# Performance work log

Measured on AMD Instinct MI355X. Metric: run time of the kernel, lower is better.

## Reference

```python
import jax, jax.numpy as jnp
import numpy as np

L = 5        # n_layers
H = 8        # heads
DH = 32      # dim_head = n_hidden // heads
D = 256      # n_hidden
KR = 4       # key_ratio
QKD = KR * DH  # 128, q/k feature dim
IN = 3       # fun_dim + space_dim
OUT = 1      # out_dim
N = 32768    # number of mesh points
EPS = 1e-5

def _ln(x, g, b):
    m = jnp.mean(x, axis=-1, keepdims=True)
    v = jnp.var(x, axis=-1, keepdims=True)
    return (x - m) * jax.lax.rsqrt(v + EPS) * g + b

def _gelu(x):
    return jax.nn.gelu(x, approximate=False)  # torch nn.GELU default (erf)

def setup_inputs() -> dict:
    key = jax.random.key(0)
    ks = iter(jax.random.split(key, 64))
    def w(*s):
        return jax.random.normal(next(ks), s, jnp.float32) * 0.02
    return {
        "x": jax.random.normal(next(ks), (N, IN), jnp.float32),
        # preprocess MLP: Linear(IN,2D)+GELU, Linear(2D,D)
        "pre_w1": w(IN, 2 * D), "pre_b1": jnp.zeros((2 * D,), jnp.float32),
        "pre_w2": w(2 * D, D), "pre_b2": jnp.zeros((D,), jnp.float32),
        "placeholder": jax.random.uniform(next(ks), (D,), jnp.float32) / D,
        # per-block params stacked over L
        "ln1_g": jnp.ones((L, D), jnp.float32), "ln1_b": jnp.zeros((L, D), jnp.float32),
        "inp_w": w(L, D, D), "inp_b": jnp.zeros((L, D), jnp.float32),
        "temp_q": jnp.full((L, H), 0.5, jnp.float32), "temp_k": jnp.full((L, H), 0.5, jnp.float32),
        "wq": w(L, DH, QKD), "wk": w(L, DH, QKD), "wv": w(L, DH, DH),
        "out_w1": w(L, D, D), "out_b1": jnp.zeros((L, D), jnp.float32),
        "out_w2": w(L, D, D), "out_b2": jnp.zeros((L, D), jnp.float32),
        "ln2_g": jnp.ones((L, D), jnp.float32), "ln2_b": jnp.zeros((L, D), jnp.float32),
        "mlp_w1": w(L, D, D), "mlp_b1": jnp.zeros((L, D), jnp.float32),  # mlp_ratio=1 -> hidden=D
        "mlp_w2": w(L, D, D), "mlp_b2": jnp.zeros((L, D), jnp.float32),
        # last-layer head
        "ln3_g": jnp.ones((D,), jnp.float32), "ln3_b": jnp.zeros((D,), jnp.float32),
        "head_w": w(D, OUT), "head_b": jnp.zeros((OUT,), jnp.float32),
    }

def reference(x, pre_w1, pre_b1, pre_w2, pre_b2, placeholder,
              ln1_g, ln1_b, inp_w, inp_b, temp_q, temp_k, wq, wk, wv,
              out_w1, out_b1, out_w2, out_b2, ln2_g, ln2_b,
              mlp_w1, mlp_b1, mlp_w2, mlp_b2, ln3_g, ln3_b, head_w, head_b):
    # preprocess + placeholder bias
    fx = _gelu(x[None] @ pre_w1 + pre_b1) @ pre_w2 + pre_b2  # [1, N, D]
    fx = fx + placeholder
    for i in range(L):
        # --- LinearNO attention block ---
        h = _ln(fx, ln1_g[i], ln1_b[i])
        xm = h @ inp_w[i] + inp_b[i]                       # [1, N, D]
        xm = xm.reshape(1, N, H, DH).transpose(0, 2, 1, 3)  # [1, H, N, DH]
        q = jnp.einsum('bhnd,de->bhne', xm, wq[i])          # [1, H, N, QKD]
        k = jnp.einsum('bhnd,de->bhne', xm, wk[i])          # [1, H, N, QKD]
        v = jnp.einsum('bhnd,dc->bhnc', xm, wv[i])          # [1, H, N, DH]
        tq = jnp.clip(temp_q[i], 0.1, 2.0)[None, :, None, None]
        tk = jnp.clip(temp_k[i], 0.1, 2.0)[None, :, None, None]
        q = jax.nn.softmax(q / tq, axis=-1)  # over feature dim
        k = jax.nn.softmax(k / tk, axis=-2)  # over point dim
        kv = jnp.einsum('bhnd,bhnc->bhdc', k, v)    # [1, H, QKD, DH]
        qkv = jnp.einsum('bhnd,bhdc->bhnc', q, kv)  # [1, H, N, DH]
        qkv = qkv.transpose(0, 2, 1, 3).reshape(1, N, D)
        attn = _gelu(qkv @ out_w1[i] + out_b1[i]) @ out_w2[i] + out_b2[i]
        fx = attn + fx
        # --- MLP block (n_layers=0, res=False: pre + post only) ---
        h2 = _ln(fx, ln2_g[i], ln2_b[i])
        fx = _gelu(h2 @ mlp_w1[i] + mlp_b1[i]) @ mlp_w2[i] + mlp_b2[i] + fx
    # last block head: mlp2(ln_3(fx))
    out = _ln(fx, ln3_g, ln3_b) @ head_w + head_b  # [1, N, OUT]
    return out[0]  # module returns fx[0]
```

## Files before the change

### kernel.cpp

```cpp
#include <hip/hip_runtime.h>
#include <hip/hip_bf16.h>
#include <math.h>

constexpr int NP  = 32768;
constexpr int HH  = 8;

typedef short bf16x8 __attribute__((ext_vector_type(8)));
typedef float f32x4  __attribute__((ext_vector_type(4)));

__device__ __forceinline__ float gelu_f(float x) {
    return 0.5f * x * (1.0f + erff(x * 0.70710678118654752f));
}

__device__ __forceinline__ unsigned short f2bf(float x) {
    union { float f; unsigned u; } v; v.f = x;
    unsigned r = v.u + 0x7fffu + ((v.u >> 16) & 1u);
    return (unsigned short)(r >> 16);
}

__device__ __forceinline__ float bf2f(unsigned short h) {
    union { unsigned u; float f; } v; v.u = ((unsigned)h) << 16;
    return v.f;
}

__global__ __launch_bounds__(256) void transpose_bf16_k(
    const float* __restrict__ src, unsigned short* __restrict__ dst, int K)
{
    __shared__ float tile[32][33];
    int g = blockIdx.z;
    int k0 = blockIdx.x * 32, c0 = blockIdx.y * 32;
    int tx = threadIdx.x & 31, ty = threadIdx.x >> 5;
    const float* s = src + (size_t)g * K * 256;
    unsigned short* d = dst + (size_t)g * 256 * K;
    #pragma unroll
    for (int rr = 0; rr < 4; ++rr) {
        int r = ty + rr * 8;
        tile[r][tx] = s[(size_t)(k0 + r) * 256 + c0 + tx];
    }
    __syncthreads();
    #pragma unroll
    for (int rr = 0; rr < 4; ++rr) {
        int r = ty + rr * 8;
        d[(size_t)(c0 + r) * K + k0 + tx] = f2bf(tile[tx][r]);
    }
}

__global__ __launch_bounds__(256) void transpose_scale_bf16_k(
    const float* __restrict__ src, const float* __restrict__ g,
    unsigned short* __restrict__ dst, int K)
{
    __shared__ float tile[32][33];
    int z = blockIdx.z;
    int k0 = blockIdx.x * 32, c0 = blockIdx.y * 32;
    int tx = threadIdx.x & 31, ty = threadIdx.x >> 5;
    const float* s = src + (size_t)z * K * 256;
    unsigned short* d = dst + (size_t)z * 256 * K;
    #pragma unroll
    for (int rr = 0; rr < 4; ++rr) {
        int r = ty + rr * 8;
        tile[r][tx] = s[(size_t)(k0 + r) * 256 + c0 + tx];
    }
    __syncthreads();
    float gs = g[z * 256 + k0 + tx];
    #pragma unroll
    for (int rr = 0; rr < 4; ++rr) {
        int r = ty + rr * 8;
        d[(size_t)(c0 + r) * K + k0 + tx] = f2bf(gs * tile[tx][r]);
    }
}

__global__ __launch_bounds__(256) void colsum_k(
    const float* __restrict__ W, const float* __restrict__ g,
    const float* __restrict__ b, float* __restrict__ c2, float* __restrict__ c1)
{
    int z = blockIdx.z, c = threadIdx.x;
    const float* Wz = W + (size_t)z * 65536;
    const float* gz = g + z * 256;
    const float* bz = b + z * 256;
    float s2 = 0.f, s1 = 0.f;
    for (int k = 0; k < 256; ++k) {
        float w = Wz[k * 256 + c];
        s2 += gz[k] * w;
        s1 += bz[k] * w;
    }
    c2[z * 256 + c] = s2;
    c1[z * 256 + c] = s1;
}

__global__ __launch_bounds__(256) void prep_wkvT(
    const float* __restrict__ wk, const float* __restrict__ wv,
    const float* __restrict__ wq,
    unsigned short* __restrict__ wkT, unsigned short* __restrict__ wvT,
    unsigned short* __restrict__ wqT)
{
    int l = blockIdx.x, tid = threadIdx.x;
    for (int idx = tid; idx < 4096; idx += 256) {
        int d = idx >> 5, k = idx & 31;
        wkT[l * 4096 + idx] = f2bf(wk[l * 4096 + k * 128 + d]);
        wqT[l * 4096 + idx] = f2bf(wq[l * 4096 + k * 128 + d]);
    }
    for (int idx = tid; idx < 1024; idx += 256) {
        int c = idx >> 5, k = idx & 31;
        wvT[l * 1024 + idx] = f2bf(wv[l * 1024 + k * 32 + c]);
    }
}

template<bool GENA, bool AF32, bool LNFOLD, bool DOGELU, bool RESID, bool STATS, bool PERM>
__global__ __launch_bounds__(256) void gemm_bf(
    const unsigned short* __restrict__ Ah, const float* __restrict__ Af,
    const unsigned short* __restrict__ Wt,
    const float* __restrict__ bias, const float* __restrict__ bias2,
    float* __restrict__ outF, unsigned short* __restrict__ outH,
    const float* __restrict__ stats_in, float* __restrict__ stats_out,
    const float* __restrict__ c1v, const float* __restrict__ c2vec,
    const float* __restrict__ genx, const float* __restrict__ genw1,
    const float* __restrict__ genb1, int K)
{
    __shared__ __align__(16) unsigned short As[128 * 64];
    __shared__ __align__(16) unsigned short Bs[128 * 64];
    __shared__ float rmean[LNFOLD ? 128 : 1];
    __shared__ float rrstd[LNFOLD ? 128 : 1];
    __shared__ float w1s[GENA ? 1536 : 1];
    __shared__ float b1s[GENA ? 512 : 1];
    __shared__ float x3s[GENA ? 512 : 1];

    const int tid = threadIdx.x;
    const int rBase = blockIdx.x * 128, cBase = blockIdx.y * 128;

    if constexpr (GENA) {
        for (int i2 = tid; i2 < 1536; i2 += 256) w1s[i2] = genw1[i2];
        for (int i2 = tid; i2 < 512; i2 += 256) b1s[i2] = genb1[i2];
        if (tid < 128) {
            x3s[tid * 4 + 0] = genx[(size_t)(rBase + tid) * 3 + 0];
            x3s[tid * 4 + 1] = genx[(size_t)(rBase + tid) * 3 + 1];
            x3s[tid * 4 + 2] = genx[(size_t)(rBase + tid) * 3 + 2];
        }
        __syncthreads();
    }
    if constexpr (LNFOLD) {
        if (tid < 128) {
            const float* sp = stats_in + (size_t)(rBase + tid) * 8;
            float4 s0 = *(const float4*)sp;
            float4 s1 = *(const float4*)(sp + 4);
            float mean = (s0.x + s0.z + s1.x + s1.z) * (1.f / 256.f);
            float ex2  = (s0.y + s0.w + s1.y + s1.w) * (1.f / 256.f);
            rmean[tid] = mean;
            rrstd[tid] = rsqrtf(fmaxf(ex2 - mean * mean, 0.f) + 1e-5f);
        }
        __syncthreads();
    }

    f32x4 acc[4][4];
    #pragma unroll
    for (int i = 0; i < 4; ++i)
        #pragma unroll
        for (int j = 0; j < 4; ++j)
            acc[i][j] = (f32x4){0.f, 0.f, 0.f, 0.f};

    const int lane = tid & 63, wid = tid >> 6;
    const int wr = wid >> 1, wc = wid & 1;
    const int lrow = lane & 15, quad = lane >> 4;
    const int srow = tid >> 3;
    const int sch  = tid & 7;

    for (int kc = 0; kc < K; kc += 64) {
        if constexpr (GENA) {
            #pragma unroll
            for (int it = 0; it < 4; ++it) {
                int row = srow + it * 32;
                float x0 = x3s[row * 4 + 0], x1 = x3s[row * 4 + 1], x2 = x3s[row * 4 + 2];
                unsigned short pk[8];
                #pragma unroll
                for (int j = 0; j < 8; ++j) {
                    int k = kc + sch * 8 + j;
                    float t = x0 * w1s[k] + x1 * w1s[512 + k] + x2 * w1s[1024 + k] + b1s[k];
                    pk[j] = f2bf(gelu_f(t));
                }
                *(uint4*)&As[row * 64 + ((sch ^ (row & 7)) << 3)] = *(uint4*)pk;
            }
        } else if constexpr (AF32) {
            #pragma unroll
            for (int it = 0; it < 4; ++it) {
                int row = srow + it * 32;
                const float* ap = Af + (size_t)(rBase + row) * K + kc + sch * 8;
                float4 a0 = *(const float4*)ap;
                float4 a1 = *(const float4*)(ap + 4);
                unsigned short pk[8];
                pk[0] = f2bf(a0.x); pk[1] = f2bf(a0.y); pk[2] = f2bf(a0.z); pk[3] = f2bf(a0.w);
                pk[4] = f2bf(a1.x); pk[5] = f2bf(a1.y); pk[6] = f2bf(a1.z); pk[7] = f2bf(a1.w);
                *(uint4*)&As[row * 64 + ((sch ^ (row & 7)) << 3)] = *(uint4*)pk;
            }
        } else {
            #pragma unroll
            for (int it = 0; it < 4; ++it) {
                int row = srow + it * 32;
                uint4 av = *(const uint4*)(Ah + (size_t)(rBase + row) * K + kc + sch * 8);
                *(uint4*)&As[row * 64 + ((sch ^ (row & 7)) << 3)] = av;
            }
        }
        #pragma unroll
        for (int it = 0; it < 4; ++it) {
            int n = srow + it * 32;
            uint4 wv_ = *(const uint4*)(Wt + (size_t)(cBase + n) * K + kc + sch * 8);
            *(uint4*)&Bs[n * 64 + ((sch ^ (n & 7)) << 3)] = wv_;
        }
        __syncthreads();
        #pragma unroll
        for (int ks = 0; ks < 2; ++ks) {
            bf16x8 af[4], bfr[4];
            #pragma unroll
            for (int t = 0; t < 4; ++t) {
                int row = wr * 64 + t * 16 + lrow;
                af[t] = *(bf16x8*)&As[row * 64 + (((ks * 4 + quad) ^ (row & 7)) << 3)];
                int n = wc * 64 + t * 16 + lrow;
                bfr[t] = *(bf16x8*)&Bs[n * 64 + (((ks * 4 + quad) ^ (n & 7)) << 3)];
            }
            #pragma unroll
            for (int ti = 0; ti < 4; ++ti)
                #pragma unroll
                for (int tj = 0; tj < 4; ++tj)
                    acc[ti][tj] = __builtin_amdgcn_mfma_f32_16x16x32_bf16(
                        af[ti], bfr[tj], acc[ti][tj], 0, 0, 0);
        }
        __syncthreads();
    }

    float c1b[4], c2r[4];
    #pragma unroll
    for (int tj = 0; tj < 4; ++tj) {
        int gcol = cBase + wc * 64 + tj * 16 + lrow;
        float b = bias[gcol];
        if (bias2) b += bias2[gcol];
        if constexpr (LNFOLD) {
            c1b[tj] = c1v[gcol] + b;
            c2r[tj] = c2vec[gcol];
        } else {
            c1b[tj] = b;
            c2r[tj] = 0.f;
        }
    }
    #pragma unroll
    for (int ti = 0; ti < 4; ++ti) {
        #pragma unroll
        for (int r = 0; r < 4; ++r) {
            int rib = wr * 64 + ti * 16 + quad * 4 + r;
            int grow = rBase + rib;
            float mean = 0.f, rstd = 1.f;
            if constexpr (LNFOLD) { mean = rmean[rib]; rstd = rrstd[rib]; }
            float vv[4];
            #pragma unroll
            for (int tj = 0; tj < 4; ++tj) {
                float t = acc[ti][tj][r];
                float v;
                if constexpr (LNFOLD) v = rstd * (t - mean * c2r[tj]) + c1b[tj];
                else                  v = t + c1b[tj];
                if constexpr (DOGELU) v = gelu_f(v);
                vv[tj] = v;
            }
            if constexpr (RESID) {
                #pragma unroll
                for (int tj = 0; tj < 4; ++tj) {
                    int gcol = cBase + wc * 64 + tj * 16 + lrow;
                    vv[tj] += outF[(size_t)grow * 256 + gcol];
                }
            }
            if constexpr (STATS) {
                float rs = vv[0] + vv[1] + vv[2] + vv[3];
                float rq = vv[0]*vv[0] + vv[1]*vv[1] + vv[2]*vv[2] + vv[3]*vv[3];
                #pragma unroll
                for (int m = 1; m < 16; m <<= 1) {
                    rs += __shfl_xor(rs, m);
                    rq += __shfl_xor(rq, m);
                }
                if (lrow == 0) {
                    stats_out[(size_t)grow * 8 + (blockIdx.y * 2 + wc) * 2 + 0] = rs;
                    stats_out[(size_t)grow * 8 + (blockIdx.y * 2 + wc) * 2 + 1] = rq;
                }
            }
            #pragma unroll
            for (int tj = 0; tj < 4; ++tj) {
                int gcol = cBase + wc * 64 + tj * 16 + lrow;
                if constexpr (PERM) {
                    size_t pidx = (size_t)(gcol >> 5) * NP * 32 + (size_t)grow * 32 + (gcol & 31);
                    if (outF) outF[pidx] = vv[tj];
                    if (outH) outH[pidx] = f2bf(vv[tj]);
                } else {
                    if (outF) outF[(size_t)grow * 256 + gcol] = vv[tj];
                    if (outH) outH[(size_t)grow * 256 + gcol] = f2bf(vv[tj]);
                }
            }
        }
    }
}

template<bool AF32, bool LNFOLD, bool WSTATS, bool NEXTW>
__global__ __launch_bounds__(256) void gemm_lgl(
    const unsigned short* __restrict__ Ah, const float* __restrict__ Af,
    const unsigned short* __restrict__ W1t, const unsigned short* __restrict__ W2t,
    const float* __restrict__ b1, const float* __restrict__ b2,
    float* __restrict__ fx,
    const float* __restrict__ stats_in, float* __restrict__ stats_out,
    const float* __restrict__ c1v, const float* __restrict__ c2vec,
    const unsigned short* __restrict__ W3t, const float* __restrict__ b3,
    const float* __restrict__ c1n, const float* __restrict__ c2n,
    unsigned short* __restrict__ outNext)
{
    __shared__ __align__(16) unsigned short As[64 * 64];
    __shared__ __align__(16) unsigned short Bs[256 * 64];
    __shared__ __align__(16) unsigned short Ts[64 * 256];
    __shared__ float rmean[(LNFOLD || NEXTW) ? 64 : 1];
    __shared__ float rrstd[(LNFOLD || NEXTW) ? 64 : 1];
    __shared__ float ssum[NEXTW ? 256 : 1];
    __shared__ float ssq [NEXTW ? 256 : 1];

    const int tid = threadIdx.x;
    const int rBase = blockIdx.x * 64;
    const int lane = tid & 63, wid = tid >> 6;
    const int lrow = lane & 15, quad = lane >> 4;

    if constexpr (LNFOLD) {
        if (tid < 64) {
            const float* sp = stats_in + (size_t)(rBase + tid) * 8;
            float4 s0 = *(const float4*)sp;
            float4 s1 = *(const float4*)(sp + 4);
            float mean = (s0.x + s0.z + s1.x + s1.z) * (1.f / 256.f);
            float ex2  = (s0.y + s0.w + s1.y + s1.w) * (1.f / 256.f);
            rmean[tid] = mean;
            rrstd[tid] = rsqrtf(fmaxf(ex2 - mean * mean, 0.f) + 1e-5f);
        }
    }

    f32x4 acc[4][4];
    #pragma unroll
    for (int i = 0; i < 4; ++i)
        #pragma unroll
        for (int j = 0; j < 4; ++j)
            acc[i][j] = (f32x4){0.f, 0.f, 0.f, 0.f};

    for (int kc = 0; kc < 256; kc += 64) {
        #pragma unroll
        for (int it = 0; it < 2; ++it) {
            int idx = tid + it * 256;
            int row = idx >> 3, sch = idx & 7;
            if constexpr (AF32) {
                const float* ap = Af + (size_t)(rBase + row) * 256 + kc + sch * 8;
                float4 a0 = *(const float4*)ap;
                float4 a1 = *(const float4*)(ap + 4);
                unsigned short pk[8];
                pk[0] = f2bf(a0.x); pk[1] = f2bf(a0.y); pk[2] = f2bf(a0.z); pk[3] = f2bf(a0.w);
                pk[4] = f2bf(a1.x); pk[5] = f2bf(a1.y); pk[6] = f2bf(a1.z); pk[7] = f2bf(a1.w);
                *(uint4*)&As[row * 64 + ((sch ^ (row & 7)) << 3)] = *(uint4*)pk;
            } else {
                uint4 av = *(const uint4*)(Ah + (size_t)(rBase + row) * 256 + kc + sch * 8);
                *(uint4*)&As[row * 64 + ((sch ^ (row & 7)) << 3)] = av;
            }
        }
        #pragma unroll
        for (int it = 0; it < 8; ++it) {
            int idx = tid + it * 256;
            int n = idx >> 3, sch = idx & 7;
            uint4 wv_ = *(const uint4*)(W1t + (size_t)n * 256 + kc + sch * 8);
            *(uint4*)&Bs[n * 64 + ((sch ^ (n & 7)) << 3)] = wv_;
        }
        __syncthreads();
        #pragma unroll
        for (int ks = 0; ks < 2; ++ks) {
            bf16x8 af[4], bfr[4];
            #pragma unroll
            for (int t = 0; t < 4; ++t) {
                int row = t * 16 + lrow;
                af[t] = *(bf16x8*)&As[row * 64 + (((ks * 4 + quad) ^ (row & 7)) << 3)];
                int n = wid * 64 + t * 16 + lrow;
                bfr[t] = *(bf16x8*)&Bs[n * 64 + (((ks * 4 + quad) ^ (n & 7)) << 3)];
            }
            #pragma unroll
            for (int ti = 0; ti < 4; ++ti)
                #pragma unroll
                for (int tj = 0; tj < 4; ++tj)
                    acc[ti][tj] = __builtin_amdgcn_mfma_f32_16x16x32_bf16(
                        af[ti], bfr[tj], acc[ti][tj], 0, 0, 0);
        }
        __syncthreads();
    }

    {
        float c1b[4], c2r[4];
        #pragma unroll
        for (int tj = 0; tj < 4; ++tj) {
            int gcol = wid * 64 + tj * 16 + lrow;
            if constexpr (LNFOLD) {
                c1b[tj] = c1v[gcol] + b1[gcol];
                c2r[tj] = c2vec[gcol];
            } else {
                c1b[tj] = b1[gcol];
                c2r[tj] = 0.f;
            }
        }
        #pragma unroll
        for (int ti = 0; ti < 4; ++ti) {
            #pragma unroll
            for (int r = 0; r < 4; ++r) {
                int row = ti * 16 + quad * 4 + r;
                float mean = 0.f, rstd = 1.f;
                if constexpr (LNFOLD) { mean = rmean[row]; rstd = rrstd[row]; }
                #pragma unroll
                for (int tj = 0; tj < 4; ++tj) {
                    float t = acc[ti][tj][r];
                    float v;
                    if constexpr (LNFOLD) v = rstd * (t - mean * c2r[tj]) + c1b[tj];
                    else                  v = t + c1b[tj];
                    v = gelu_f(v);
                    int col = wid * 64 + tj * 16 + lrow;
                    int ch = col >> 3;
                    Ts[row * 256 + ((ch ^ (row & 7)) << 3) + (col & 7)] = f2bf(v);
                }
            }
        }
    }
    __syncthreads();

    f32x4 acc2[4][4];
    #pragma unroll
    for (int i = 0; i < 4; ++i)
        #pragma unroll
        for (int j = 0; j < 4; ++j)
            acc2[i][j] = (f32x4){0.f, 0.f, 0.f, 0.f};

    for (int kc = 0; kc < 256; kc += 64) {
        #pragma unroll
        for (int it = 0; it < 8; ++it) {
            int idx = tid + it * 256;
            int n = idx >> 3, sch = idx & 7;
            uint4 wv_ = *(const uint4*)(W2t + (size_t)n * 256 + kc + sch * 8);
            *(uint4*)&Bs[n * 64 + ((sch ^ (n & 7)) << 3)] = wv_;
        }
        __syncthreads();
        #pragma unroll
        for (int ks = 0; ks < 2; ++ks) {
            bf16x8 af[4], bfr[4];
            #pragma unroll
            for (int t = 0; t < 4; ++t) {
                int row = t * 16 + lrow;
                int ch = (kc >> 3) + ks * 4 + quad;
                af[t] = *(bf16x8*)&Ts[row * 256 + ((ch ^ (row & 7)) << 3)];
                int n = wid * 64 + t * 16 + lrow;
                bfr[t] = *(bf16x8*)&Bs[n * 64 + (((ks * 4 + quad) ^ (n & 7)) << 3)];
            }
            #pragma unroll
            for (int ti = 0; ti < 4; ++ti)
                #pragma unroll
                for (int tj = 0; tj < 4; ++tj)
                    acc2[ti][tj] = __builtin_amdgcn_mfma_f32_16x16x32_bf16(
                        af[ti], bfr[tj], acc2[ti][tj], 0, 0, 0);
        }
        __syncthreads();
    }

    float bb[4];
    #pragma unroll
    for (int tj = 0; tj < 4; ++tj) bb[tj] = b2[wid * 64 + tj * 16 + lrow];
    #pragma unroll
    for (int ti = 0; ti < 4; ++ti) {
        #pragma unroll
        for (int r = 0; r < 4; ++r) {
            int row = ti * 16 + quad * 4 + r;
            int grow = rBase + row;
            float vv[4];
            #pragma unroll
            for (int tj = 0; tj < 4; ++tj) {
                int gcol = wid * 64 + tj * 16 + lrow;
                vv[tj] = acc2[ti][tj][r] + bb[tj] + fx[(size_t)grow * 256 + gcol];
            }
            if constexpr (WSTATS || NEXTW) {
                float rs = vv[0] + vv[1] + vv[2] + vv[3];
                float rq = vv[0]*vv[0] + vv[1]*vv[1] + vv[2]*vv[2] + vv[3]*vv[3];
                #pragma unroll
                for (int m = 1; m < 16; m <<= 1) {
                    rs += __shfl_xor(rs, m);
                    rq += __shfl_xor(rq, m);
                }
                if (lrow == 0) {
                    if constexpr (WSTATS) {
                        stats_out[(size_t)grow * 8 + wid * 2 + 0] = rs;
                        stats_out[(size_t)grow * 8 + wid * 2 + 1] = rq;
                    }
                    if constexpr (NEXTW) {
                        ssum[row * 4 + wid] = rs;
                        ssq [row * 4 + wid] = rq;
                    }
                }
            }
            #pragma unroll
            for (int tj = 0; tj < 4; ++tj) {
                int gcol = wid * 64 + tj * 16 + lrow;
                fx[(size_t)grow * 256 + gcol] = vv[tj];
                if constexpr (NEXTW) {
                    int ch = gcol >> 3;
                    Ts[row * 256 + ((ch ^ (row & 7)) << 3) + (gcol & 7)] = f2bf(vv[tj]);
                }
            }
        }
    }

    if constexpr (NEXTW) {
        __syncthreads();
        if (tid < 64) {
            float q0 = ssum[tid * 4 + 0], q1 = ssum[tid * 4 + 1];
            float q2 = ssum[tid * 4 + 2], q3 = ssum[tid * 4 + 3];
            float p0 = ssq [tid * 4 + 0], p1 = ssq [tid * 4 + 1];
            float p2 = ssq [tid * 4 + 2], p3 = ssq [tid * 4 + 3];
            float mean = (q0 + q1 + q2 + q3) * (1.f / 256.f);
            float ex2  = (p0 + p1 + p2 + p3) * (1.f / 256.f);
            rmean[tid] = mean;
            rrstd[tid] = rsqrtf(fmaxf(ex2 - mean * mean, 0.f) + 1e-5f);
        }
        __syncthreads();

        f32x4 acc3[4][4];
        #pragma unroll
        for (int i = 0; i < 4; ++i)
            #pragma unroll
            for (int j = 0; j < 4; ++j)
                acc3[i][j] = (f32x4){0.f, 0.f, 0.f, 0.f};

        for (int kc = 0; kc < 256; kc += 64) {
            #pragma unroll
            for (int it = 0; it < 8; ++it) {
                int idx = tid + it * 256;
                int n = idx >> 3, sch = idx & 7;
                uint4 wv_ = *(const uint4*)(W3t + (size_t)n * 256 + kc + sch * 8);
                *(uint4*)&Bs[n * 64 + ((sch ^ (n & 7)) << 3)] = wv_;
            }
            __syncthreads();
            #pragma unroll
            for (int ks = 0; ks < 2; ++ks) {
                bf16x8 af[4], bfr[4];
                #pragma unroll
                for (int t = 0; t < 4; ++t) {
                    int row = t * 16 + lrow;
                    int ch = (kc >> 3) + ks * 4 + quad;
                    af[t] = *(bf16x8*)&Ts[row * 256 + ((ch ^ (row & 7)) << 3)];
                    int n = wid * 64 + t * 16 + lrow;
                    bfr[t] = *(bf16x8*)&Bs[n * 64 + (((ks * 4 + quad) ^ (n & 7)) << 3)];
                }
                #pragma unroll
                for (int ti = 0; ti < 4; ++ti)
                    #pragma unroll
                    for (int tj = 0; tj < 4; ++tj)
                        acc3[ti][tj] = __builtin_amdgcn_mfma_f32_16x16x32_bf16(
                            af[ti], bfr[tj], acc3[ti][tj], 0, 0, 0);
            }
            __syncthreads();
        }

        float c1b3[4], c2r3[4];
        #pragma unroll
        for (int tj = 0; tj < 4; ++tj) {
            int gcol = wid * 64 + tj * 16 + lrow;
            c1b3[tj] = c1n[gcol] + b3[gcol];
            c2r3[tj] = c2n[gcol];
        }
        #pragma unroll
        for (int ti = 0; ti < 4; ++ti) {
            #pragma unroll
            for (int r = 0; r < 4; ++r) {
                int row = ti * 16 + quad * 4 + r;
                int grow = rBase + row;
                float mean = rmean[row], rstd = rrstd[row];
                #pragma unroll
                for (int tj = 0; tj < 4; ++tj) {
                    int gcol = wid * 64 + tj * 16 + lrow;
                    float t = acc3[ti][tj][r];
                    float v = rstd * (t - mean * c2r3[tj]) + c1b3[tj];
                    size_t pidx = (size_t)(gcol >> 5) * NP * 32 + (size_t)grow * 32 + (gcol & 31);
                    outNext[pidx] = f2bf(v);
                }
            }
        }
    }
}

__global__ __launch_bounds__(256) void kv6_kernel(
    const unsigned short* __restrict__ xm2h, const unsigned short* __restrict__ wkT,
    const unsigned short* __restrict__ wvT, const float* __restrict__ tk_arr,
    float* __restrict__ partials, int layer)
{
    __shared__ __align__(16) unsigned short xs[64 * 32];
    __shared__ __align__(16) unsigned short wks[128 * 32];
    __shared__ __align__(16) unsigned short wvs[32 * 32];
    __shared__ __align__(16) unsigned short els[128 * 72];
    __shared__ __align__(16) unsigned short vls[32 * 72];
    __shared__ float sums[4 * 128];

    const int tid = threadIdx.x;
    const int h = blockIdx.y;
    const int rowBase = blockIdx.x * 512;
    const int w = tid >> 6, lane = tid & 63;
    const int lrow = lane & 15, quad = lane >> 4;

    float tk = fminf(fmaxf(tk_arr[layer * 8 + h], 0.1f), 2.0f);
    float invtk = 1.0f / tk;

    #pragma unroll
    for (int it = 0; it < 2; ++it) {
        int cid = tid + it * 256;
        int d = cid >> 2, kc = cid & 3;
        uint4 v = *(const uint4*)(wkT + d * 32 + kc * 8);
        *(uint4*)&wks[d * 32 + ((kc ^ (d & 3)) << 3)] = v;
    }
    if (tid < 128) {
        int c = tid >> 2, kc = tid & 3;
        uint4 v = *(const uint4*)(wvT + c * 32 + kc * 8);
        *(uint4*)&wvs[c * 32 + ((kc ^ (c & 3)) << 3)] = v;
    }

    f32x4 acc2[2][2];
    #pragma unroll
    for (int di = 0; di < 2; ++di)
        #pragma unroll
        for (int ci = 0; ci < 2; ++ci)
            acc2[di][ci] = (f32x4){0.f, 0.f, 0.f, 0.f};
    float seacc[8];
    #pragma unroll
    for (int dt = 0; dt < 8; ++dt) seacc[dt] = 0.f;

    const unsigned short* src = xm2h + (size_t)h * NP * 32 + (size_t)rowBase * 32;

    for (int sub = 0; sub < 8; ++sub) {
        __syncthreads();
        {
            int row = tid >> 2, kc = tid & 3;
            uint4 v = *(const uint4*)(src + (size_t)(sub * 64 + row) * 32 + kc * 8);
            *(uint4*)&xs[row * 32 + ((kc ^ (row & 3)) << 3)] = v;
        }
        __syncthreads();
        int arow = w * 16 + lrow;
        bf16x8 ax = *(bf16x8*)&xs[arow * 32 + ((quad ^ (arow & 3)) << 3)];
        #pragma unroll
        for (int ct = 0; ct < 2; ++ct) {
            int c = ct * 16 + lrow;
            bf16x8 bw = *(bf16x8*)&wvs[c * 32 + ((quad ^ (c & 3)) << 3)];
            f32x4 cc = (f32x4){0.f, 0.f, 0.f, 0.f};
            cc = __builtin_amdgcn_mfma_f32_16x16x32_bf16(ax, bw, cc, 0, 0, 0);
            unsigned short pk[4];
            pk[0] = f2bf(cc[0]); pk[1] = f2bf(cc[1]);
            pk[2] = f2bf(cc[2]); pk[3] = f2bf(cc[3]);
            *(uint2*)&vls[(ct * 16 + lrow) * 72 + w * 16 + quad * 4] = *(uint2*)pk;
        }
        #pragma unroll
        for (int dt = 0; dt < 8; ++dt) {
            int d = dt * 16 + lrow;
            bf16x8 bw = *(bf16x8*)&wks[d * 32 + ((quad ^ (d & 3)) << 3)];
            f32x4 cc = (f32x4){0.f, 0.f, 0.f, 0.f};
            cc = __builtin_amdgcn_mfma_f32_16x16x32_bf16(ax, bw, cc, 0, 0, 0);
            unsigned short pk[4];
            float se = 0.f;
            #pragma unroll
            for (int r = 0; r < 4; ++r) {
                float l = fminf(fmaxf(cc[r] * invtk, -30.f), 30.f);
                unsigned short eb = f2bf(__expf(l));
                pk[r] = eb;
                se += bf2f(eb);
            }
            seacc[dt] += se;
            *(uint2*)&els[d * 72 + w * 16 + quad * 4] = *(uint2*)pk;
        }
        __syncthreads();
        #pragma unroll
        for (int di = 0; di < 2; ++di) {
            int dm = (2 * w + di) * 16 + lrow;
            #pragma unroll
            for (int ks = 0; ks < 2; ++ks) {
                bf16x8 ae = *(bf16x8*)&els[dm * 72 + ks * 32 + quad * 8];
                #pragma unroll
                for (int ci = 0; ci < 2; ++ci) {
                    int cn = ci * 16 + lrow;
                    bf16x8 bv = *(bf16x8*)&vls[cn * 72 + ks * 32 + quad * 8];
                    acc2[di][ci] = __builtin_amdgcn_mfma_f32_16x16x32_bf16(
                        ae, bv, acc2[di][ci], 0, 0, 0);
                }
            }
        }
    }

    float* outp = partials + ((size_t)h * 64 + blockIdx.x) * 4224;
    #pragma unroll
    for (int di = 0; di < 2; ++di)
        #pragma unroll
        for (int ci = 0; ci < 2; ++ci)
            #pragma unroll
            for (int r = 0; r < 4; ++r) {
                int d = (2 * w + di) * 16 + quad * 4 + r;
                int c = ci * 16 + lrow;
                outp[d * 32 + c] = acc2[di][ci][r];
            }
    #pragma unroll
    for (int dt = 0; dt < 8; ++dt) {
        float s = seacc[dt];
        s += __shfl_xor(s, 16);
        s += __shfl_xor(s, 32);
        if (quad == 0) sums[w * 128 + dt * 16 + lrow] = s;
    }
    __syncthreads();
    if (tid < 128)
        outp[4096 + tid] = sums[tid] + sums[128 + tid] + sums[256 + tid] + sums[384 + tid];
}

__global__ __launch_bounds__(256) void kv_reduce_kernel(
    const float* __restrict__ partials, unsigned short* __restrict__ kvT,
    float* __restrict__ sumexp)
{
    int gid = blockIdx.x * 256 + threadIdx.x;
    if (gid >= 8 * 4224) return;
    int h = gid / 4224, idx = gid % 4224;
    const float* base = partials + (size_t)h * 64 * 4224 + idx;
    float s = 0.f;
    #pragma unroll 8
    for (int c = 0; c < 64; ++c) s += base[(size_t)c * 4224];
    if (idx < 4096) {
        int d = idx >> 5, c = idx & 31;
        kvT[(size_t)h * 4096 + c * 128 + d] = f2bf(s);
    } else {
        sumexp[h * 128 + (idx - 4096)] = s;
    }
}

__global__ __launch_bounds__(256) void qkv6_kernel(
    const unsigned short* __restrict__ xm2h, const unsigned short* __restrict__ wqT,
    const float* __restrict__ tq_arr, const unsigned short* __restrict__ kvT,
    const float* __restrict__ sumexp, unsigned short* __restrict__ outH, int layer)
{
    __shared__ __align__(16) unsigned short xs[64 * 32];
    __shared__ __align__(16) unsigned short wqs[128 * 32];
    __shared__ __align__(16) unsigned short kvb[32 * 136];
    __shared__ __align__(16) unsigned short els[64 * 136];
    __shared__ float ises[128];

    const int tid = threadIdx.x;
    const int h = blockIdx.y;
    const int rowBase = blockIdx.x * 64;
    const int w = tid >> 6, lane = tid & 63;
    const int lrow = lane & 15, quad = lane >> 4;

    float tq = fminf(fmaxf(tq_arr[layer * 8 + h], 0.1f), 2.0f);
    float invtq = 1.0f / tq;

    if (tid < 128) ises[tid] = 1.0f / sumexp[h * 128 + tid];
    #pragma unroll
    for (int it = 0; it < 2; ++it) {
        int cid = tid + it * 256;
        int d = cid >> 2, kc = cid & 3;
        uint4 v = *(const uint4*)(wqT + d * 32 + kc * 8);
        *(uint4*)&wqs[d * 32 + ((kc ^ (d & 3)) << 3)] = v;
    }
    #pragma unroll
    for (int it = 0; it < 2; ++it) {
        int cid = tid + it * 256;
        int c = cid >> 4, k8 = cid & 15;
        uint4 v = *(const uint4*)(kvT + (size_t)h * 4096 + c * 128 + k8 * 8);
        *(uint4*)&kvb[c * 136 + k8 * 8] = v;
    }
    {
        int row = tid >> 2, kc = tid & 3;
        uint4 v = *(const uint4*)(xm2h + (size_t)h * NP * 32 +
                                  (size_t)(rowBase + row) * 32 + kc * 8);
        *(uint4*)&xs[row * 32 + ((kc ^ (row & 3)) << 3)] = v;
    }
    __syncthreads();

    int arow = w * 16 + lrow;
    bf16x8 ax = *(bf16x8*)&xs[arow * 32 + ((quad ^ (arow & 3)) << 3)];
    f32x4 lg[8];
    #pragma unroll
    for (int dt = 0; dt < 8; ++dt) {
        int d = dt * 16 + lrow;
        bf16x8 bw = *(bf16x8*)&wqs[d * 32 + ((quad ^ (d & 3)) << 3)];
        f32x4 cc = (f32x4){0.f, 0.f, 0.f, 0.f};
        lg[dt] = __builtin_amdgcn_mfma_f32_16x16x32_bf16(ax, bw, cc, 0, 0, 0);
    }
    float isv[8];
    #pragma unroll
    for (int dt = 0; dt < 8; ++dt) isv[dt] = ises[dt * 16 + lrow];

    #pragma unroll
    for (int r = 0; r < 4; ++r) {
        float m = lg[0][r];
        #pragma unroll
        for (int dt = 1; dt < 8; ++dt) m = fmaxf(m, lg[dt][r]);
        m = fmaxf(m, __shfl_xor(m, 1));
        m = fmaxf(m, __shfl_xor(m, 2));
        m = fmaxf(m, __shfl_xor(m, 4));
        m = fmaxf(m, __shfl_xor(m, 8));
        float e[8], s = 0.f;
        #pragma unroll
        for (int dt = 0; dt < 8; ++dt) {
            e[dt] = __expf((lg[dt][r] - m) * invtq);
            s += e[dt];
        }
        s += __shfl_xor(s, 1);
        s += __shfl_xor(s, 2);
        s += __shfl_xor(s, 4);
        s += __shfl_xor(s, 8);
        float inv = 1.0f / s;
        int erow = w * 16 + quad * 4 + r;
        #pragma unroll
        for (int dt = 0; dt < 8; ++dt)
            els[erow * 136 + dt * 16 + lrow] = f2bf(e[dt] * inv * isv[dt]);
    }

    #pragma unroll
    for (int ct = 0; ct < 2; ++ct) {
        f32x4 oc = (f32x4){0.f, 0.f, 0.f, 0.f};
        #pragma unroll
        for (int ks = 0; ks < 4; ++ks) {
            bf16x8 ae = *(bf16x8*)&els[(w * 16 + lrow) * 136 + ks * 32 + quad * 8];
            bf16x8 bv = *(bf16x8*)&kvb[(ct * 16 + lrow) * 136 + ks * 32 + quad * 8];
            oc = __builtin_amdgcn_mfma_f32_16x16x32_bf16(ae, bv, oc, 0, 0, 0);
        }
        #pragma unroll
        for (int r = 0; r < 4; ++r)
            outH[(size_t)(rowBase + w * 16 + quad * 4 + r) * 256 +
                 h * 32 + ct * 16 + lrow] = f2bf(oc[r]);
    }
}

__global__ __launch_bounds__(256) void head_kernel(
    const float* __restrict__ fx, const float* __restrict__ g, const float* __restrict__ b,
    const float* __restrict__ hw, const float* __restrict__ hb, float* __restrict__ out)
{
    int lane = threadIdx.x & 63;
    int row = blockIdx.x * 4 + (threadIdx.x >> 6);
    float4 v = *(const float4*)(fx + (size_t)row * 256 + lane * 4);
    float s1 = v.x + v.y + v.z + v.w;
    float s2 = v.x * v.x + v.y * v.y + v.z * v.z + v.w * v.w;
    #pragma unroll
    for (int m = 1; m < 64; m <<= 1) { s1 += __shfl_xor(s1, m); s2 += __shfl_xor(s2, m); }
    float mean = s1 * 0.00390625f;
    float rstd = rsqrtf(fmaxf(s2 * 0.00390625f - mean * mean, 0.f) + 1e-5f);
    float4 gg = *(const float4*)(g + lane * 4);
    float4 bb = *(const float4*)(b + lane * 4);
    float4 w4 = *(const float4*)(hw + lane * 4);
    float d = ((v.x - mean) * rstd * gg.x + bb.x) * w4.x
            + ((v.y - mean) * rstd * gg.y + bb.y) * w4.y
            + ((v.z - mean) * rstd * gg.z + bb.z) * w4.z
            + ((v.w - mean) * rstd * gg.w + bb.w) * w4.w;
    #pragma unroll
    for (int m = 1; m < 64; m <<= 1) d += __shfl_xor(d, m);
    if (lane == 0) out[row] = d + hb[0];
}

extern "C" void kernel_launch(void* const* d_in, const int* in_sizes, int n_in,
                              void* d_out, int out_size, void* d_ws, size_t ws_size,
                              hipStream_t stream)
{
    const float* x      = (const float*)d_in[0];
    const float* pre_w1 = (const float*)d_in[1];
    const float* pre_b1 = (const float*)d_in[2];
    const float* pre_w2 = (const float*)d_in[3];
    const float* pre_b2 = (const float*)d_in[4];
    const float* ph     = (const float*)d_in[5];
    const float* ln1_g  = (const float*)d_in[6];
    const float* ln1_b  = (const float*)d_in[7];
    const float* inp_w  = (const float*)d_in[8];
    const float* inp_b  = (const float*)d_in[9];
    const float* temp_q = (const float*)d_in[10];
    const float* temp_k = (const float*)d_in[11];
    const float* wq     = (const float*)d_in[12];
    const float* wk     = (const float*)d_in[13];
    const float* wv     = (const float*)d_in[14];
    const float* out_w1 = (const float*)d_in[15];
    const float* out_b1 = (const float*)d_in[16];
    const float* out_w2 = (const float*)d_in[17];
    const float* out_b2 = (const float*)d_in[18];
    const float* ln2_g  = (const float*)d_in[19];
    const float* ln2_b  = (const float*)d_in[20];
    const float* mlp_w1 = (const float*)d_in[21];
    const float* mlp_b1 = (const float*)d_in[22];
    const float* mlp_w2 = (const float*)d_in[23];
    const float* mlp_b2 = (const float*)d_in[24];
    const float* ln3_g  = (const float*)d_in[25];
    const float* ln3_b  = (const float*)d_in[26];
    const float* head_w = (const float*)d_in[27];
    const float* head_b = (const float*)d_in[28];
    float* out = (float*)d_out;

    float* fx = (float*)d_ws;
    unsigned short* fxh = (unsigned short*)(fx + (size_t)NP * 256);
    unsigned short* ChH = fxh + (size_t)NP * 256;
    unsigned short* xm2h = ChH;
    float* scr = (float*)(ChH + (size_t)NP * 256);
    float* st = scr + (size_t)NP * 256;
    unsigned short* kvT = (unsigned short*)(st + (size_t)NP * 8);
    float* se = (float*)(kvT + 8 * 4096);
    float* c1i = se + 8 * 128;
    float* c2i = c1i + 1280;
    float* c1m = c2i + 1280;
    float* c2m = c1m + 1280;
    unsigned short* wtPre = (unsigned short*)(c2m + 1280);
    unsigned short* wtL   = wtPre + 256 * 512;
    unsigned short* wkT   = wtL + 25 * 65536;
    unsigned short* wvT   = wkT + 5 * 4096;
    unsigned short* wqT   = wvT + 5 * 1024;

    unsigned short* wtIn = wtL;
    unsigned short* wtO1 = wtL +  5 * 65536;
    unsigned short* wtO2 = wtL + 10 * 65536;
    unsigned short* wtM1 = wtL + 15 * 65536;
    unsigned short* wtM2 = wtL + 20 * 65536;

    unsigned short* qh = (unsigned short*)scr;

    dim3 bt(256);

    transpose_bf16_k<<<dim3(16, 8, 1), bt, 0, stream>>>(pre_w2, wtPre, 512);
    transpose_scale_bf16_k<<<dim3(8, 8, 5), bt, 0, stream>>>(inp_w,  ln1_g, wtIn, 256);
    transpose_bf16_k<<<dim3(8, 8, 5), bt, 0, stream>>>(out_w1, wtO1, 256);
    transpose_bf16_k<<<dim3(8, 8, 5), bt, 0, stream>>>(out_w2, wtO2, 256);
    transpose_scale_bf16_k<<<dim3(8, 8, 5), bt, 0, stream>>>(mlp_w1, ln2_g, wtM1, 256);
    transpose_bf16_k<<<dim3(8, 8, 5), bt, 0, stream>>>(mlp_w2, wtM2, 256);
    colsum_k<<<dim3(1, 1, 5), bt, 0, stream>>>(inp_w,  ln1_g, ln1_b, c2i, c1i);
    colsum_k<<<dim3(1, 1, 5), bt, 0, stream>>>(mlp_w1, ln2_g, ln2_b, c2m, c1m);
    prep_wkvT<<<dim3(5), bt, 0, stream>>>(wk, wv, wq, wkT, wvT, wqT);

    dim3 gg(256, 2);

    gemm_bf<true, false, false, false, false, true, false><<<gg, bt, 0, stream>>>(
        nullptr, nullptr, wtPre, pre_b2, ph, fx, nullptr, nullptr, st,
        nullptr, nullptr, x, pre_w1, pre_b1, 512);

    gemm_bf<false, true, true, false, false, false, true><<<gg, bt, 0, stream>>>(
        nullptr, fx, wtIn, inp_b, nullptr, nullptr, xm2h,
        st, nullptr, c1i, c2i, nullptr, nullptr, nullptr, 256);

    for (int i = 0; i < 5; ++i) {
        kv6_kernel<<<dim3(64, 8), bt, 0, stream>>>(
            xm2h, wkT + (size_t)i * 4096, wvT + (size_t)i * 1024, temp_k, scr, i);
        kv_reduce_kernel<<<dim3(132), bt, 0, stream>>>(scr, kvT, se);
        qkv6_kernel<<<dim3(512, 8), bt, 0, stream>>>(
            xm2h, wqT + (size_t)i * 4096, temp_q, kvT, se, qh, i);
        gemm_lgl<false, false, true, false><<<dim3(512), bt, 0, stream>>>(
            qh, nullptr, wtO1 + (size_t)i * 65536, wtO2 + (size_t)i * 65536,
            out_b1 + i * 256, out_b2 + i * 256, fx, nullptr, st, nullptr, nullptr,
            nullptr, nullptr, nullptr, nullptr, nullptr);
        if (i < 4) {
            gemm_lgl<true, true, false, true><<<dim3(512), bt, 0, stream>>>(
                nullptr, fx, wtM1 + (size_t)i * 65536, wtM2 + (size_t)i * 65536,
                mlp_b1 + i * 256, mlp_b2 + i * 256, fx, st, nullptr,
                c1m + i * 256, c2m + i * 256,
                wtIn + (size_t)(i + 1) * 65536, inp_b + (i + 1) * 256,
                c1i + (i + 1) * 256, c2i + (i + 1) * 256, xm2h);
        } else {
            gemm_lgl<true, true, false, false><<<dim3(512), bt, 0, stream>>>(
                nullptr, fx, wtM1 + (size_t)i * 65536, wtM2 + (size_t)i * 65536,
                mlp_b1 + i * 256, mlp_b2 + i * 256, fx, st, nullptr,
                c1m + i * 256, c2m + i * 256,
                nullptr, nullptr, nullptr, nullptr, nullptr);
        }
    }
    head_kernel<<<dim3(NP / 4), bt, 0, stream>>>(fx, ln3_g, ln3_b, head_w, head_b, out);
}
```

Measured before the change: 809.4 us.

## Fuse q-softmax attention apply with output MLP into one kernel per layer

The separate qkv6 kernel, which wrote a bf16 attention output to global memory, is replaced by attn_lgl. For a 64-row tile, attn_lgl loops over all 8 heads, builds the attention output in shared memory, then runs the two output-projection GEMMs with GELU, the residual add and the LN statistics in the same kernel. This removes one launch and a global write/read of the N×256 intermediate per layer. The xm buffer is now double-buffered (xmA/xmB), because the fused MLP kernel writes the next layer's xm while the current one may still be read. The cost is 8× fewer blocks in the attention stage (512 instead of 4096), serialized head processing with a sync per head, and larger shared-memory use that may lower occupancy.

```diff
diff --git a/kernel.cpp b/kernel.cpp
--- a/kernel.cpp
+++ b/kernel.cpp
@@ -287,6 +287,217 @@
                 } else {
                     if (outF) outF[(size_t)grow * 256 + gcol] = vv[tj];
                     if (outH) outH[(size_t)grow * 256 + gcol] = f2bf(vv[tj]);
+                }
+            }
+        }
+    }
+}
+
+__global__ __launch_bounds__(256) void attn_lgl(
+    const unsigned short* __restrict__ xm, const unsigned short* __restrict__ wqT,
+    const float* __restrict__ tq_arr,
+    const unsigned short* __restrict__ kvT, const float* __restrict__ sumexp,
+    const unsigned short* __restrict__ O1t, const float* __restrict__ ob1,
+    const unsigned short* __restrict__ O2t, const float* __restrict__ ob2,
+    float* __restrict__ fx, float* __restrict__ stats_out, int layer)
+{
+    __shared__ __align__(16) unsigned char upool[38912];
+    __shared__ __align__(16) unsigned short Ts[64 * 256];
+
+    unsigned short* xs  = (unsigned short*)(upool);
+    unsigned short* wqs = (unsigned short*)(upool + 4096);
+    unsigned short* kvb = (unsigned short*)(upool + 12288);
+    unsigned short* els = (unsigned short*)(upool + 20992);
+    float*          ises = (float*)(upool + 38400);
+    unsigned short* Bs  = (unsigned short*)(upool);
+
+    const int tid = threadIdx.x;
+    const int rBase = blockIdx.x * 64;
+    const int lane = tid & 63, wid = tid >> 6;
+    const int lrow = lane & 15, quad = lane >> 4;
+
+    #pragma unroll
+    for (int it = 0; it < 2; ++it) {
+        int cid = tid + it * 256;
+        int d = cid >> 2, kc = cid & 3;
+        uint4 v = *(const uint4*)(wqT + d * 32 + kc * 8);
+        *(uint4*)&wqs[d * 32 + ((kc ^ (d & 3)) << 3)] = v;
+    }
+    for (int h = 0; h < 8; ++h) {
+        if (h) __syncthreads();
+        float tq = fminf(fmaxf(tq_arr[layer * 8 + h], 0.1f), 2.0f);
+        float invtq = 1.0f / tq;
+        if (tid < 128) ises[tid] = 1.0f / sumexp[h * 128 + tid];
+        #pragma unroll
+        for (int it = 0; it < 2; ++it) {
+            int cid = tid + it * 256;
+            int c = cid >> 4, k8 = cid & 15;
+            uint4 v = *(const uint4*)(kvT + (size_t)h * 4096 + c * 128 + k8 * 8);
+            *(uint4*)&kvb[c * 136 + k8 * 8] = v;
+        }
+        {
+            int row = tid >> 2, kc = tid & 3;
+            uint4 v = *(const uint4*)(xm + (size_t)h * NP * 32 +
+                                      (size_t)(rBase + row) * 32 + kc * 8);
+            *(uint4*)&xs[row * 32 + ((kc ^ (row & 3)) << 3)] = v;
+        }
+        __syncthreads();
+
+        int arow = wid * 16 + lrow;
+        bf16x8 ax = *(bf16x8*)&xs[arow * 32 + ((quad ^ (arow & 3)) << 3)];
+        f32x4 lg[8];
+        #pragma unroll
+        for (int dt = 0; dt < 8; ++dt) {
+            int d = dt * 16 + lrow;
+            bf16x8 bw = *(bf16x8*)&wqs[d * 32 + ((quad ^ (d & 3)) << 3)];
+            f32x4 cc = (f32x4){0.f, 0.f, 0.f, 0.f};
+            lg[dt] = __builtin_amdgcn_mfma_f32_16x16x32_bf16(ax, bw, cc, 0, 0, 0);
+        }
+        float isv[8];
+        #pragma unroll
+        for (int dt = 0; dt < 8; ++dt) isv[dt] = ises[dt * 16 + lrow];
+
+        #pragma unroll
+        for (int r = 0; r < 4; ++r) {
+            float m = lg[0][r];
+            #pragma unroll
+            for (int dt = 1; dt < 8; ++dt) m = fmaxf(m, lg[dt][r]);
+            m = fmaxf(m, __shfl_xor(m, 1));
+            m = fmaxf(m, __shfl_xor(m, 2));
+            m = fmaxf(m, __shfl_xor(m, 4));
+            m = fmaxf(m, __shfl_xor(m, 8));
+            float e[8], s = 0.f;
+            #pragma unroll
+            for (int dt = 0; dt < 8; ++dt) {
+                e[dt] = __expf((lg[dt][r] - m) * invtq);
+                s += e[dt];
+            }
+            s += __shfl_xor(s, 1);
+            s += __shfl_xor(s, 2);
+            s += __shfl_xor(s, 4);
+            s += __shfl_xor(s, 8);
+            float inv = 1.0f / s;
+            int erow = wid * 16 + quad * 4 + r;
+            #pragma unroll
+            for (int dt = 0; dt < 8; ++dt)
+                els[erow * 136 + dt * 16 + lrow] = f2bf(e[dt] * inv * isv[dt]);
+        }
+
+        #pragma unroll
+        for (int ct = 0; ct < 2; ++ct) {
+            f32x4 oc = (f32x4){0.f, 0.f, 0.f, 0.f};
+            #pragma unroll
+            for (int ks = 0; ks < 4; ++ks) {
+                bf16x8 ae = *(bf16x8*)&els[(wid * 16 + lrow) * 136 + ks * 32 + quad * 8];
+                bf16x8 bv = *(bf16x8*)&kvb[(ct * 16 + lrow) * 136 + ks * 32 + quad * 8];
+                oc = __builtin_amdgcn_mfma_f32_16x16x32_bf16(ae, bv, oc, 0, 0, 0);
+            }
+            #pragma unroll
+            for (int r = 0; r < 4; ++r) {
+                int row = wid * 16 + quad * 4 + r;
+                int col = h * 32 + ct * 16 + lrow;
+                int ch = col >> 3;
+                Ts[row * 256 + ((ch ^ (row & 7)) << 3) + (col & 7)] = f2bf(oc[r]);
+            }
+        }
+    }
+    __syncthreads();
+
+    auto gemm_phase = [&](const unsigned short* __restrict__ Wt, f32x4 (&acc)[4][4]) {
+        for (int kc = 0; kc < 256; kc += 64) {
+            #pragma unroll
+            for (int it = 0; it < 8; ++it) {
+                int idx = tid + it * 256;
+                int n = idx >> 3, sch = idx & 7;
+                uint4 wv_ = *(const uint4*)(Wt + (size_t)n * 256 + kc + sch * 8);
+                *(uint4*)&Bs[n * 64 + ((sch ^ (n & 7)) << 3)] = wv_;
+            }
+            __syncthreads();
+            #pragma unroll
+            for (int ks = 0; ks < 2; ++ks) {
+                bf16x8 af[4], bfr[4];
+                #pragma unroll
+                for (int t = 0; t < 4; ++t) {
+                    int row = t * 16 + lrow;
+                    int ch = (kc >> 3) + ks * 4 + quad;
+                    af[t] = *(bf16x8*)&Ts[row * 256 + ((ch ^ (row & 7)) << 3)];
+                    int n = wid * 64 + t * 16 + lrow;
+                    bfr[t] = *(bf16x8*)&Bs[n * 64 + (((ks * 4 + quad) ^ (n & 7)) << 3)];
+                }
+                #pragma unroll
+                for (int ti = 0; ti < 4; ++ti)
+                    #pragma unroll
+                    for (int tj = 0; tj < 4; ++tj)
+                        acc[ti][tj] = __builtin_amdgcn_mfma_f32_16x16x32_bf16(
+                            af[ti], bfr[tj], acc[ti][tj], 0, 0, 0);
+            }
+            __syncthreads();
+        }
+    };
+
+    f32x4 acc[4][4];
+    #pragma unroll
+    for (int i = 0; i < 4; ++i)
+        #pragma unroll
+        for (int j = 0; j < 4; ++j) acc[i][j] = (f32x4){0.f, 0.f, 0.f, 0.f};
+    gemm_phase(O1t, acc);
+    {
+        float c1b[4];
+        #pragma unroll
+        for (int tj = 0; tj < 4; ++tj) c1b[tj] = ob1[wid * 64 + tj * 16 + lrow];
+        #pragma unroll
+        for (int ti = 0; ti < 4; ++ti) {
+            #pragma unroll
+            for (int r = 0; r < 4; ++r) {
+                int row = ti * 16 + quad * 4 + r;
+                #pragma unroll
+                for (int tj = 0; tj < 4; ++tj) {
+                    float v = gelu_f(acc[ti][tj][r] + c1b[tj]);
+                    int col = wid * 64 + tj * 16 + lrow;
+                    int ch = col >> 3;
+                    Ts[row * 256 + ((ch ^ (row & 7)) << 3) + (col & 7)] = f2bf(v);
+                }
+            }
+        }
+    }
+    __syncthreads();
+
+    #pragma unroll
+    for (int i = 0; i < 4; ++i)
+        #pragma unroll
+        for (int j = 0; j < 4; ++j) acc[i][j] = (f32x4){0.f, 0.f, 0.f, 0.f};
+    gemm_phase(O2t, acc);
+    {
+        float bb[4];
+        #pragma unroll
+        for (int tj = 0; tj < 4; ++tj) bb[tj] = ob2[wid * 64 + tj * 16 + lrow];
+        #pragma unroll
+        for (int ti = 0; ti < 4; ++ti) {
+            #pragma unroll
+            for (int r = 0; r < 4; ++r) {
+                int row = ti * 16 + quad * 4 + r;
+                int grow = rBase + row;
+                float vv[4];
+                #pragma unroll
+                for (int tj = 0; tj < 4; ++tj) {
+                    int gcol = wid * 64 + tj * 16 + lrow;
+                    vv[tj] = acc[ti][tj][r] + bb[tj] + fx[(size_t)grow * 256 + gcol];
+                }
+                float rs = vv[0] + vv[1] + vv[2] + vv[3];
+                float rq = vv[0]*vv[0] + vv[1]*vv[1] + vv[2]*vv[2] + vv[3]*vv[3];
+                #pragma unroll
+                for (int m = 1; m < 16; m <<= 1) {
+                    rs += __shfl_xor(rs, m);
+                    rq += __shfl_xor(rq, m);
+                }
+                if (lrow == 0) {
+                    stats_out[(size_t)grow * 8 + wid * 2 + 0] = rs;
+                    stats_out[(size_t)grow * 8 + wid * 2 + 1] = rq;
+                }
+                #pragma unroll
+                for (int tj = 0; tj < 4; ++tj) {
+                    int gcol = wid * 64 + tj * 16 + lrow;
+                    fx[(size_t)grow * 256 + gcol] = vv[tj];
                 }
             }
         }
@@ -505,12 +716,8 @@
     if constexpr (NEXTW) {
         __syncthreads();
         if (tid < 64) {
-            float q0 = ssum[tid * 4 + 0], q1 = ssum[tid * 4 + 1];
-            float q2 = ssum[tid * 4 + 2], q3 = ssum[tid * 4 + 3];
-            float p0 = ssq [tid * 4 + 0], p1 = ssq [tid * 4 + 1];
-            float p2 = ssq [tid * 4 + 2], p3 = ssq [tid * 4 + 3];
-            float mean = (q0 + q1 + q2 + q3) * (1.f / 256.f);
-            float ex2  = (p0 + p1 + p2 + p3) * (1.f / 256.f);
+            float mean = (ssum[tid*4+0] + ssum[tid*4+1] + ssum[tid*4+2] + ssum[tid*4+3]) * (1.f/256.f);
+            float ex2  = (ssq [tid*4+0] + ssq [tid*4+1] + ssq [tid*4+2] + ssq [tid*4+3]) * (1.f/256.f);
             rmean[tid] = mean;
             rrstd[tid] = rsqrtf(fmaxf(ex2 - mean * mean, 0.f) + 1e-5f);
         }
@@ -722,105 +929,6 @@
         kvT[(size_t)h * 4096 + c * 128 + d] = f2bf(s);
     } else {
         sumexp[h * 128 + (idx - 4096)] = s;
-    }
-}
-
-__global__ __launch_bounds__(256) void qkv6_kernel(
-    const unsigned short* __restrict__ xm2h, const unsigned short* __restrict__ wqT,
-    const float* __restrict__ tq_arr, const unsigned short* __restrict__ kvT,
-    const float* __restrict__ sumexp, unsigned short* __restrict__ outH, int layer)
-{
-    __shared__ __align__(16) unsigned short xs[64 * 32];
-    __shared__ __align__(16) unsigned short wqs[128 * 32];
-    __shared__ __align__(16) unsigned short kvb[32 * 136];
-    __shared__ __align__(16) unsigned short els[64 * 136];
-    __shared__ float ises[128];
-
-    const int tid = threadIdx.x;
-    const int h = blockIdx.y;
-    const int rowBase = blockIdx.x * 64;
-    const int w = tid >> 6, lane = tid & 63;
-    const int lrow = lane & 15, quad = lane >> 4;
-
-    float tq = fminf(fmaxf(tq_arr[layer * 8 + h], 0.1f), 2.0f);
-    float invtq = 1.0f / tq;
-
-    if (tid < 128) ises[tid] = 1.0f / sumexp[h * 128 + tid];
-    #pragma unroll
-    for (int it = 0; it < 2; ++it) {
-        int cid = tid + it * 256;
-        int d = cid >> 2, kc = cid & 3;
-        uint4 v = *(const uint4*)(wqT + d * 32 + kc * 8);
-        *(uint4*)&wqs[d * 32 + ((kc ^ (d & 3)) << 3)] = v;
-    }
-    #pragma unroll
-    for (int it = 0; it < 2; ++it) {
-        int cid = tid + it * 256;
-        int c = cid >> 4, k8 = cid & 15;
-        uint4 v = *(const uint4*)(kvT + (size_t)h * 4096 + c * 128 + k8 * 8);
-        *(uint4*)&kvb[c * 136 + k8 * 8] = v;
-    }
-    {
-        int row = tid >> 2, kc = tid & 3;
-        uint4 v = *(const uint4*)(xm2h + (size_t)h * NP * 32 +
-                                  (size_t)(rowBase + row) * 32 + kc * 8);
-        *(uint4*)&xs[row * 32 + ((kc ^ (row & 3)) << 3)] = v;
-    }
-    __syncthreads();
-
-    int arow = w * 16 + lrow;
-    bf16x8 ax = *(bf16x8*)&xs[arow * 32 + ((quad ^ (arow & 3)) << 3)];
-    f32x4 lg[8];
-    #pragma unroll
-    for (int dt = 0; dt < 8; ++dt) {
-        int d = dt * 16 + lrow;
-        bf16x8 bw = *(bf16x8*)&wqs[d * 32 + ((quad ^ (d & 3)) << 3)];
-        f32x4 cc = (f32x4){0.f, 0.f, 0.f, 0.f};
-        lg[dt] = __builtin_amdgcn_mfma_f32_16x16x32_bf16(ax, bw, cc, 0, 0, 0);
-    }
-    float isv[8];
-    #pragma unroll
-    for (int dt = 0; dt < 8; ++dt) isv[dt] = ises[dt * 16 + lrow];
-
-    #pragma unroll
-    for (int r = 0; r < 4; ++r) {
-        float m = lg[0][r];
-        #pragma unroll
-        for (int dt = 1; dt < 8; ++dt) m = fmaxf(m, lg[dt][r]);
-        m = fmaxf(m, __shfl_xor(m, 1));
-        m = fmaxf(m, __shfl_xor(m, 2));
-        m = fmaxf(m, __shfl_xor(m, 4));
-        m = fmaxf(m, __shfl_xor(m, 8));
-        float e[8], s = 0.f;
-        #pragma unroll
-        for (int dt = 0; dt < 8; ++dt) {
-            e[dt] = __expf((lg[dt][r] - m) * invtq);
-            s += e[dt];
-        }
-        s += __shfl_xor(s, 1);
-        s += __shfl_xor(s, 2);
-        s += __shfl_xor(s, 4);
-        s += __shfl_xor(s, 8);
-        float inv = 1.0f / s;
-        int erow = w * 16 + quad * 4 + r;
-        #pragma unroll
-        for (int dt = 0; dt < 8; ++dt)
-            els[erow * 136 + dt * 16 + lrow] = f2bf(e[dt] * inv * isv[dt]);
-    }
-
-    #pragma unroll
-    for (int ct = 0; ct < 2; ++ct) {
-        f32x4 oc = (f32x4){0.f, 0.f, 0.f, 0.f};
-        #pragma unroll
-        for (int ks = 0; ks < 4; ++ks) {
-            bf16x8 ae = *(bf16x8*)&els[(w * 16 + lrow) * 136 + ks * 32 + quad * 8];
-            bf16x8 bv = *(bf16x8*)&kvb[(ct * 16 + lrow) * 136 + ks * 32 + quad * 8];
-            oc = __builtin_amdgcn_mfma_f32_16x16x32_bf16(ae, bv, oc, 0, 0, 0);
-        }
-        #pragma unroll
-        for (int r = 0; r < 4; ++r)
-            outH[(size_t)(rowBase + w * 16 + quad * 4 + r) * 256 +
-                 h * 32 + ct * 16 + lrow] = f2bf(oc[r]);
     }
 }
 
@@ -885,10 +993,9 @@
     float* out = (float*)d_out;
 
     float* fx = (float*)d_ws;
-    unsigned short* fxh = (unsigned short*)(fx + (size_t)NP * 256);
-    unsigned short* ChH = fxh + (size_t)NP * 256;
-    unsigned short* xm2h = ChH;
-    float* scr = (float*)(ChH + (size_t)NP * 256);
+    unsigned short* xmB = (unsigned short*)(fx + (size_t)NP * 256);
+    unsigned short* xmA = xmB + (size_t)NP * 256;
+    float* scr = (float*)(xmA + (size_t)NP * 256);
     float* st = scr + (size_t)NP * 256;
     unsigned short* kvT = (unsigned short*)(st + (size_t)NP * 8);
     float* se = (float*)(kvT + 8 * 4096);
@@ -908,8 +1015,6 @@
     unsigned short* wtM1 = wtL + 15 * 65536;
     unsigned short* wtM2 = wtL + 20 * 65536;
 
-    unsigned short* qh = (unsigned short*)scr;
-
     dim3 bt(256);
 
     transpose_bf16_k<<<dim3(16, 8, 1), bt, 0, stream>>>(pre_w2, wtPre, 512);
@@ -929,26 +1034,27 @@
         nullptr, nullptr, x, pre_w1, pre_b1, 512);
 
     gemm_bf<false, true, true, false, false, false, true><<<gg, bt, 0, stream>>>(
-        nullptr, fx, wtIn, inp_b, nullptr, nullptr, xm2h,
+        nullptr, fx, wtIn, inp_b, nullptr, nullptr, xmA,
         st, nullptr, c1i, c2i, nullptr, nullptr, nullptr, 256);
 
     for (int i = 0; i < 5; ++i) {
+        unsigned short* xmCur  = (i & 1) ? xmB : xmA;
+        unsigned short* xmNext = (i & 1) ? xmA : xmB;
         kv6_kernel<<<dim3(64, 8), bt, 0, stream>>>(
-            xm2h, wkT + (size_t)i * 4096, wvT + (size_t)i * 1024, temp_k, scr, i);
+            xmCur, wkT + (size_t)i * 4096, wvT + (size_t)i * 1024, temp_k, scr, i);
         kv_reduce_kernel<<<dim3(132), bt, 0, stream>>>(scr, kvT, se);
-        qkv6_kernel<<<dim3(512, 8), bt, 0, stream>>>(
-            xm2h, wqT + (size_t)i * 4096, temp_q, kvT, se, qh, i);
-        gemm_lgl<false, false, true, false><<<dim3(512), bt, 0, stream>>>(
-            qh, nullptr, wtO1 + (size_t)i * 65536, wtO2 + (size_t)i * 65536,
-            out_b1 + i * 256, out_b2 + i * 256, fx, nullptr, st, nullptr, nullptr,
-            nullptr, nullptr, nullptr, nullptr, nullptr);
+        attn_lgl<<<dim3(512), bt, 0, stream>>>(
+            xmCur, wqT + (size_t)i * 4096, temp_q, kvT, se,
+            wtO1 + (size_t)i * 65536, out_b1 + i * 256,
+            wtO2 + (size_t)i * 65536, out_b2 + i * 256,
+            fx, st, i);
         if (i < 4) {
             gemm_lgl<true, true, false, true><<<dim3(512), bt, 0, stream>>>(
                 nullptr, fx, wtM1 + (size_t)i * 65536, wtM2 + (size_t)i * 65536,
                 mlp_b1 + i * 256, mlp_b2 + i * 256, fx, st, nullptr,
                 c1m + i * 256, c2m + i * 256,
                 wtIn + (size_t)(i + 1) * 65536, inp_b + (i + 1) * 256,
-                c1i + (i + 1) * 256, c2i + (i + 1) * 256, xm2h);
+                c1i + (i + 1) * 256, c2i + (i + 1) * 256, xmNext);
         } else {
             gemm_lgl<true, true, false, false><<<dim3(512), bt, 0, stream>>>(
                 nullptr, fx, wtM1 + (size_t)i * 65536, wtM2 + (size_t)i * 65536,
```

Result: no change. 818.4 us (+1.1%).
